# Kernel tuning notes

Hardware: AMD Instinct MI355X
Metric: run time of the kernel (lower is better)

## Reference

```python
import jax, jax.numpy as jnp
import numpy as np

B, T, E, D = 8, 2048, 2048, 256  # batch, seq (== max_seq_len), embed_size, block_size

def setup_inputs() -> dict:
    key = jax.random.key(0)
    kx, kq, kk, kv = jax.random.split(key, 4)
    x = jax.random.normal(kx, (B, T, E), dtype=jnp.float32)
    s = 1.0 / np.sqrt(E)
    Wq = jax.random.normal(kq, (E, D), dtype=jnp.float32) * s
    Wk = jax.random.normal(kk, (E, D), dtype=jnp.float32) * s
    Wv = jax.random.normal(kv, (E, D), dtype=jnp.float32) * s
    return {"x": x, "Wq": Wq, "Wk": Wk, "Wv": Wv}

def reference(x, Wq, Wk, Wv):
    # q,k,v: [B, T, D]
    q = jnp.einsum('bte,ed->btd', x, Wq)
    k = jnp.einsum('bte,ed->btd', x, Wk)
    v = jnp.einsum('bte,ed->btd', x, Wv)
    scores = jnp.einsum('bqd,bkd->bqk', q, k)  # [B, T, T]
    causal = jnp.tril(jnp.ones((T, T), dtype=bool))
    scores = jnp.where(causal, scores, -jnp.inf)
    inv_sqrt_d = 1.0 / np.sqrt(D).astype(np.float32)
    # Original divides by sqrt(D) twice: once before softmax, once inside -> net 1/D scale
    scores = scores * inv_sqrt_d
    attn = jax.nn.softmax(scores * inv_sqrt_d, axis=-1)
    z = jnp.einsum('bqk,bkd->bqd', attn, v)
    return z
```

## Files before the change

### kernel.cpp

```cpp
#include <hip/hip_runtime.h>
#include <hip/hip_bf16.h>

typedef unsigned short u16;
typedef unsigned int u32;
typedef __attribute__((ext_vector_type(8))) __bf16 bf16x8;
typedef __attribute__((ext_vector_type(4))) float f32x4;
typedef __attribute__((ext_vector_type(16))) float f32x16;
typedef __attribute__((ext_vector_type(2))) unsigned u32x2;

__device__ __forceinline__ u16 f2bf(float f) {
  u32 u = __builtin_bit_cast(u32, f);
  return (u16)((u + 0x7fffu + ((u >> 16) & 1u)) >> 16);
}
__device__ __forceinline__ float bf2f(u16 h) {
  u32 u = ((u32)h) << 16;
  return __builtin_bit_cast(float, u);
}
__device__ __forceinline__ u32 pk2(float lo, float hi) {
  union { __bf16 b[2]; u32 u; } r;
  r.b[0] = (__bf16)lo; r.b[1] = (__bf16)hi;
  return r.u;
}

__device__ __forceinline__ void pl32pair(u32& a, u32& b) {
#if __has_builtin(__builtin_amdgcn_permlane32_swap)
  u32x2 r = __builtin_amdgcn_permlane32_swap(a, b, 0, 0);
  a = r.x; b = r.y;
#else
  int hi = (int)((threadIdx.x & 63) >> 5);
  u32 as = __shfl_xor(a, 32), bs = __shfl_xor(b, 32);
  u32 na = hi ? bs : a;
  u32 nb = hi ? b : as;
  a = na; b = nb;
#endif
}
__device__ __forceinline__ float red_max32(float x) {
  u32 a = __builtin_bit_cast(u32, x), b = __builtin_bit_cast(u32, x);
  pl32pair(a, b);
  return fmaxf(__builtin_bit_cast(float, a), __builtin_bit_cast(float, b));
}
__device__ __forceinline__ float red_sum32(float x) {
  u32 a = __builtin_bit_cast(u32, x), b = __builtin_bit_cast(u32, x);
  pl32pair(a, b);
  return __builtin_bit_cast(float, a) + __builtin_bit_cast(float, b);
}

__global__ __launch_bounds__(256) void cast_x_kernel(const float* __restrict__ x,
                                                     u16* __restrict__ xb) {
  size_t i = ((size_t)blockIdx.x * 256 + threadIdx.x) * 8;
  float4 a = *(const float4*)(x + i);
  float4 b = *(const float4*)(x + i + 4);
  union { u16 h[8]; uint4 v; } o;
  o.h[0] = f2bf(a.x); o.h[1] = f2bf(a.y); o.h[2] = f2bf(a.z); o.h[3] = f2bf(a.w);
  o.h[4] = f2bf(b.x); o.h[5] = f2bf(b.y); o.h[6] = f2bf(b.z); o.h[7] = f2bf(b.w);
  *(uint4*)(xb + i) = o.v;
}

__global__ void cast_w_kernel(const float* __restrict__ Wq, const float* __restrict__ Wk,
                              const float* __restrict__ Wv, u16* __restrict__ wbt) {
  __shared__ float tile[32][33];
  int e0 = blockIdx.x * 32, d0 = blockIdx.y * 32, w = blockIdx.z;
  const float* W = (w == 0) ? Wq : ((w == 1) ? Wk : Wv);
  int x = threadIdx.x, y = threadIdx.y;
#pragma unroll
  for (int j = 0; j < 4; j++)
    tile[y + j * 8][x] = W[(size_t)(e0 + y + j * 8) * 256 + d0 + x];
  __syncthreads();
#pragma unroll
  for (int j = 0; j < 4; j++)
    wbt[(size_t)(w * 256 + d0 + y + j * 8) * 2048 + e0 + x] = f2bf(tile[x][y + j * 8]);
}

__global__ __launch_bounds__(256, 2) void gemm_kernel(const u16* __restrict__ A,
                                                      const u16* __restrict__ Bt,
                                                      u16* __restrict__ C) {
  __shared__ __align__(16) u16 As[3][4096];
  __shared__ __align__(16) u16 Bs[3][6144];

  int tid = threadIdx.x;
  int w = tid >> 6, l = tid & 63;
  int lr = l & 15, lg = l >> 4;
  int wm = w >> 1, wn = w & 1;

  int bid = blockIdx.x;
  int xcd = bid & 7;
  int colb = xcd >> 1;
  int rowb = ((xcd & 1) << 6) + (bid >> 3);
  int row0 = rowb * 128, col0 = colb * 192;

  int garow = w * 16 + (l >> 2);
  int scol = ((l & 3) * 8) ^ (((l >> 2) & 3) * 8);
  const u16* ga = A + (size_t)(row0 + garow) * 2048 + scol;
  const u16* gb = Bt + (size_t)(col0 + garow) * 2048 + scol;

  f32x4 acc[4][6];
#pragma unroll
  for (int m = 0; m < 4; m++)
#pragma unroll
    for (int n = 0; n < 6; n++) acc[m][n] = (f32x4){0.f, 0.f, 0.f, 0.f};

  int rcol = (lg * 8) ^ ((lr & 3) * 8);

#define STAGE3(ts, bi)                                                                 \
  {                                                                                    \
    _Pragma("unroll") for (int c = 0; c < 2; c++)                                      \
        __builtin_amdgcn_global_load_lds(                                              \
            (const __attribute__((address_space(1))) void*)(ga + (size_t)c * 64 * 2048 + (ts) * 32), \
            (__attribute__((address_space(3))) void*)&As[bi][(c * 64 + w * 16) * 32], 16, 0, 0); \
    _Pragma("unroll") for (int c = 0; c < 3; c++)                                      \
        __builtin_amdgcn_global_load_lds(                                              \
            (const __attribute__((address_space(1))) void*)(gb + (size_t)c * 64 * 2048 + (ts) * 32), \
            (__attribute__((address_space(3))) void*)&Bs[bi][(c * 64 + w * 16) * 32], 16, 0, 0); \
  }

  STAGE3(0, 0);
  STAGE3(1, 1);
  asm volatile("s_waitcnt vmcnt(5)" ::: "memory");
  __builtin_amdgcn_s_barrier();

  int bi = 0, bp = 2;
  for (int t = 0; t < 64; t++) {
    int ts = (t + 2 <= 63) ? (t + 2) : 63;
    const u16* asb = As[bi];
    const u16* bsb = Bs[bi];

    bf16x8 af[4], bfr[6];
#pragma unroll
    for (int m = 0; m < 4; m++)
      af[m] = *(const bf16x8*)&asb[(wm * 64 + m * 16 + lr) * 32 + rcol];
#pragma unroll
    for (int n = 0; n < 6; n++)
      bfr[n] = *(const bf16x8*)&bsb[(wn * 96 + n * 16 + lr) * 32 + rcol];

    STAGE3(ts, bp);

    asm volatile("s_waitcnt lgkmcnt(0)" ::: "memory");
    __builtin_amdgcn_sched_barrier(0);
    __builtin_amdgcn_s_setprio(1);
#pragma unroll
    for (int m = 0; m < 4; m++)
#pragma unroll
      for (int n = 0; n < 6; n++)
        acc[m][n] = __builtin_amdgcn_mfma_f32_16x16x32_bf16(af[m], bfr[n], acc[m][n], 0, 0, 0);
    __builtin_amdgcn_s_setprio(0);

    asm volatile("s_waitcnt vmcnt(5)" ::: "memory");
    __builtin_amdgcn_s_barrier();

    bi = (bi == 2) ? 0 : bi + 1;
    bp = (bp == 2) ? 0 : bp + 1;
  }
#undef STAGE3

  int crow = row0 + wm * 64;
  int ccol = col0 + wn * 96 + lr;
#pragma unroll
  for (int m = 0; m < 4; m++)
#pragma unroll
    for (int n = 0; n < 6; n++)
#pragma unroll
      for (int i = 0; i < 4; i++)
        C[(size_t)(crow + m * 16 + lg * 4 + i) * 768 + ccol + n * 16] = f2bf(acc[m][n][i]);
}

__global__ __launch_bounds__(256) void kfrag_kernel(const u16* __restrict__ qkv,
                                                    u16* __restrict__ kfrag) {
  __shared__ __align__(16) u16 tile[32 * 264];
  int t = threadIdx.x, kvb = blockIdx.x, b = blockIdx.y;
#pragma unroll
  for (int c = 0; c < 4; c++) {
    int m = c * 256 + t;
    int r = m >> 5, c16 = m & 31;
    bf16x8 v = *(const bf16x8*)(qkv + (size_t)(b * 2048 + kvb * 32 + r) * 768 + 256 + c16 * 8);
    *(bf16x8*)&tile[r * 264 + c16 * 8] = v;
  }
  __syncthreads();
#pragma unroll
  for (int c = 0; c < 4; c++) {
    int m = c * 256 + t;
    int t16 = m >> 6, l = m & 63;
    bf16x8 v = *(const bf16x8*)&tile[(l & 31) * 264 + t16 * 16 + (l >> 5) * 8];
    *(bf16x8*)(kfrag + ((size_t)((b * 64 + kvb) * 16 + t16) * 64 + l) * 8) = v;
  }
}

__global__ __launch_bounds__(256) void vfrag_kernel(const u16* __restrict__ qkv,
                                                    u16* __restrict__ vfrag) {
  __shared__ __align__(16) u16 tile[32 * 264];
  int t = threadIdx.x, kvb = blockIdx.x, b = blockIdx.y;
#pragma unroll
  for (int c = 0; c < 4; c++) {
    int m = c * 256 + t;
    int r = m >> 5, c16 = m & 31;
    bf16x8 v = *(const bf16x8*)(qkv + (size_t)(b * 2048 + kvb * 32 + r) * 768 + 512 + c16 * 8);
    *(bf16x8*)&tile[r * 264 + c16 * 8] = v;
  }
  __syncthreads();
#pragma unroll
  for (int c = 0; c < 4; c++) {
    int m = c * 256 + t;
    int ch = m >> 9, dblk = (m >> 6) & 7, l = m & 63;
    union { u16 h[8]; uint4 v; } o;
#pragma unroll
    for (int j = 0; j < 8; j++)
      o.h[j] = tile[(ch * 16 + (l >> 5) * 8 + j) * 264 + dblk * 32 + (l & 31)];
    *(uint4*)(vfrag + ((size_t)(((b * 64 + kvb) * 2 + ch) * 8 + dblk) * 64 + l) * 8) = o.v;
  }
}

__global__ __launch_bounds__(512, 2) void attn_kernel(const u16* __restrict__ qkv,
                                                      const u16* __restrict__ kfrag,
                                                      const u16* __restrict__ vfrag,
                                                      float* __restrict__ out) {
  __shared__ __align__(16) u16 qlds[16 * 512];
  __shared__ float facc[32][264];
  __shared__ float sm[4][32];
  __shared__ float sl[4][32];

  int tid = threadIdx.x;
  int w = tid >> 6, l = tid & 63;
  int ql = l & 31, hi = l >> 5;
  int stream = w & 3, dhalf = w >> 2;
  int bid = blockIdx.x;
  int b = bid & 7;
  int p = bid >> 3;

  for (int tile = 0; tile < 2; tile++) {
    int jt = tile ? p : (63 - p);
    int q0 = jt * 32;

    if (tile) __syncthreads();
#pragma unroll
    for (int c = 0; c < 2; c++) {
      int m = c * 512 + tid;
      int t16 = m >> 6, ll = m & 63;
      const u16* src = qkv + (size_t)(b * 2048 + q0 + (ll & 31)) * 768 + t16 * 16 + (ll >> 5) * 8;
      union { u16 h[8]; bf16x8 v; } in, ov;
      in.v = *(const bf16x8*)src;
#pragma unroll
      for (int j = 0; j < 8; j++) ov.h[j] = f2bf(bf2f(in.h[j]) * (1.0f / 256.0f));
      *(bf16x8*)&qlds[(t16 * 64 + ll) * 8] = ov.v;
    }
    __syncthreads();

    f32x16 o[4];
#pragma unroll
    for (int d = 0; d < 4; d++)
#pragma unroll
      for (int r = 0; r < 16; r++) o[d][r] = 0.f;
    float mreg = -__builtin_inff(), ell = 0.f;

    for (int jb = stream; jb <= jt; jb += 4) {
      const u16* kb = kfrag + ((size_t)(b * 64 + jb) * 16 * 64 + l) * 8;
      const u16* vb = vfrag + ((size_t)(b * 64 + jb) * 16 * 64 + l) * 8;

      f32x16 sA, sB;
#pragma unroll
      for (int r = 0; r < 16; r++) { sA[r] = 0.f; sB[r] = 0.f; }
#pragma unroll
      for (int g = 0; g < 4; g++) {
        bf16x8 k0 = *(const bf16x8*)(kb + (g * 4 + 0) * 512);
        bf16x8 k1 = *(const bf16x8*)(kb + (g * 4 + 1) * 512);
        bf16x8 k2 = *(const bf16x8*)(kb + (g * 4 + 2) * 512);
        bf16x8 k3 = *(const bf16x8*)(kb + (g * 4 + 3) * 512);
        bf16x8 q0f = *(const bf16x8*)&qlds[((g * 4 + 0) * 64 + l) * 8];
        bf16x8 q1f = *(const bf16x8*)&qlds[((g * 4 + 1) * 64 + l) * 8];
        bf16x8 q2f = *(const bf16x8*)&qlds[((g * 4 + 2) * 64 + l) * 8];
        bf16x8 q3f = *(const bf16x8*)&qlds[((g * 4 + 3) * 64 + l) * 8];
        sA = __builtin_amdgcn_mfma_f32_32x32x16_bf16(k0, q0f, sA, 0, 0, 0);
        sB = __builtin_amdgcn_mfma_f32_32x32x16_bf16(k1, q1f, sB, 0, 0, 0);
        sA = __builtin_amdgcn_mfma_f32_32x32x16_bf16(k2, q2f, sA, 0, 0, 0);
        sB = __builtin_amdgcn_mfma_f32_32x32x16_bf16(k3, q3f, sB, 0, 0, 0);
      }

      bf16x8 ve0[4], ve1[4];
#pragma unroll
      for (int dd = 0; dd < 4; dd++) {
        ve0[dd] = *(const bf16x8*)(vb + (dhalf * 4 + dd) * 512);
        ve1[dd] = *(const bf16x8*)(vb + (8 + dhalf * 4 + dd) * 512);
      }

      float s[16];
#pragma unroll
      for (int r = 0; r < 16; r++) s[r] = sA[r] + sB[r];

      if (jb == jt) {
#pragma unroll
        for (int r = 0; r < 16; r++) {
          int kv = (r & 3) + 8 * (r >> 2) + 4 * hi;
          if (kv > ql) s[r] = -__builtin_inff();
        }
      }

      float mx = s[0];
#pragma unroll
      for (int r = 1; r < 16; r++) mx = fmaxf(mx, s[r]);
      mx = red_max32(mx);
      if (__any(mx > mreg + 8.f)) {
        float mnew = fmaxf(mreg, mx);
        float sf = __expf(mreg - mnew);
        mreg = mnew;
        ell *= sf;
#pragma unroll
        for (int d = 0; d < 4; d++)
#pragma unroll
          for (int r = 0; r < 16; r++) o[d][r] *= sf;
      }
      float pr[16], ps = 0.f;
#pragma unroll
      for (int r = 0; r < 16; r++) { pr[r] = __expf(s[r] - mreg); ps += pr[r]; }
      ell += red_sum32(ps);

      u32 wv[8];
#pragma unroll
      for (int i = 0; i < 8; i++) wv[i] = pk2(pr[2 * i], pr[2 * i + 1]);
      pl32pair(wv[0], wv[2]); pl32pair(wv[1], wv[3]);
      pl32pair(wv[4], wv[6]); pl32pair(wv[5], wv[7]);
      union { u32 u[4]; bf16x8 v; } B0, B1;
      B0.u[0] = wv[0]; B0.u[1] = wv[1]; B0.u[2] = wv[2]; B0.u[3] = wv[3];
      B1.u[0] = wv[4]; B1.u[1] = wv[5]; B1.u[2] = wv[6]; B1.u[3] = wv[7];

#pragma unroll
      for (int dd = 0; dd < 4; dd++) {
        o[dd] = __builtin_amdgcn_mfma_f32_32x32x16_bf16(ve0[dd], B0.v, o[dd], 0, 0, 0);
        o[dd] = __builtin_amdgcn_mfma_f32_32x32x16_bf16(ve1[dd], B1.v, o[dd], 0, 0, 0);
      }
    }

    __syncthreads();
    if (w < 4 && l < 32) { sm[w][l] = mreg; sl[w][l] = ell; }
    __syncthreads();

    float M = fmaxf(fmaxf(sm[0][ql], sm[1][ql]), fmaxf(sm[2][ql], sm[3][ql]));
    float alpha = __expf(mreg - M);

#pragma unroll
    for (int ph = 0; ph < 4; ph++) {
      if (stream == ph) {
#pragma unroll
        for (int dd = 0; dd < 4; dd++)
#pragma unroll
          for (int rq = 0; rq < 4; rq++) {
            int base = (dhalf * 4 + dd) * 32 + 8 * rq + 4 * hi;
            f32x4 v;
#pragma unroll
            for (int i = 0; i < 4; i++) v[i] = alpha * o[dd][rq * 4 + i];
            float* fp = &facc[ql][base];
            if (ph == 0) *(f32x4*)fp = v;
            else {
              f32x4 old = *(const f32x4*)fp;
              *(f32x4*)fp = old + v;
            }
          }
      }
      __syncthreads();
    }

    int r = tid >> 4, lt = tid & 15;
    float Mr = fmaxf(fmaxf(sm[0][r], sm[1][r]), fmaxf(sm[2][r], sm[3][r]));
    float denom = 0.f;
#pragma unroll
    for (int ww = 0; ww < 4; ww++) denom += __expf(sm[ww][r] - Mr) * sl[ww][r];
    float inv = 1.0f / denom;
    float* orow = out + (size_t)(b * 2048 + q0 + r) * 256;
#pragma unroll
    for (int j = 0; j < 4; j++) {
      int c = (lt + j * 16) * 4;
      f32x4 v = *(const f32x4*)&facc[r][c];
      v[0] *= inv; v[1] *= inv; v[2] *= inv; v[3] *= inv;
      *(f32x4*)&orow[c] = v;
    }
  }
}

extern "C" void kernel_launch(void* const* d_in, const int* in_sizes, int n_in,
                              void* d_out, int out_size, void* d_ws, size_t ws_size,
                              hipStream_t stream) {
  (void)in_sizes; (void)n_in; (void)out_size; (void)ws_size;
  const float* x = (const float*)d_in[0];
  const float* Wq = (const float*)d_in[1];
  const float* Wk = (const float*)d_in[2];
  const float* Wv = (const float*)d_in[3];
  float* out = (float*)d_out;

  char* ws = (char*)d_ws;
  u16* xb  = (u16*)(ws);
  u16* wbt = (u16*)(ws + 67108864);
  u16* qkv = (u16*)(ws + 70254592);
  u16* kfrag = (u16*)(ws);
  u16* vfrag = (u16*)(ws + 8388608);

  cast_x_kernel<<<16384, 256, 0, stream>>>(x, xb);
  cast_w_kernel<<<dim3(64, 8, 3), dim3(32, 8), 0, stream>>>(Wq, Wk, Wv, wbt);
  gemm_kernel<<<512, 256, 0, stream>>>(xb, wbt, qkv);
  kfrag_kernel<<<dim3(64, 8), 256, 0, stream>>>(qkv, kfrag);
  vfrag_kernel<<<dim3(64, 8), 256, 0, stream>>>(qkv, vfrag);
  attn_kernel<<<256, 512, 0, stream>>>(qkv, kfrag, vfrag, out);
}
```

Baseline: 150.3 us.

## Split GEMM main loop into two MFMA phases; one attention tile per block

```diff
diff --git a/kernel.cpp b/kernel.cpp
--- a/kernel.cpp
+++ b/kernel.cpp
@@ -101,20 +101,23 @@
 
   int rcol = (lg * 8) ^ ((lr & 3) * 8);
 
-#define STAGE3(ts, bi)                                                                 \
+#define STAGE_A3(ts, bi)                                                               \
   {                                                                                    \
     _Pragma("unroll") for (int c = 0; c < 2; c++)                                      \
         __builtin_amdgcn_global_load_lds(                                              \
             (const __attribute__((address_space(1))) void*)(ga + (size_t)c * 64 * 2048 + (ts) * 32), \
             (__attribute__((address_space(3))) void*)&As[bi][(c * 64 + w * 16) * 32], 16, 0, 0); \
+  }
+#define STAGE_B3(ts, bi)                                                               \
+  {                                                                                    \
     _Pragma("unroll") for (int c = 0; c < 3; c++)                                      \
         __builtin_amdgcn_global_load_lds(                                              \
             (const __attribute__((address_space(1))) void*)(gb + (size_t)c * 64 * 2048 + (ts) * 32), \
             (__attribute__((address_space(3))) void*)&Bs[bi][(c * 64 + w * 16) * 32], 16, 0, 0); \
   }
 
-  STAGE3(0, 0);
-  STAGE3(1, 1);
+  STAGE_A3(0, 0); STAGE_B3(0, 0);
+  STAGE_A3(1, 1); STAGE_B3(1, 1);
   asm volatile("s_waitcnt vmcnt(5)" ::: "memory");
   __builtin_amdgcn_s_barrier();
 
@@ -124,33 +127,47 @@
     const u16* asb = As[bi];
     const u16* bsb = Bs[bi];
 
-    bf16x8 af[4], bfr[6];
-#pragma unroll
-    for (int m = 0; m < 4; m++)
-      af[m] = *(const bf16x8*)&asb[(wm * 64 + m * 16 + lr) * 32 + rcol];
+    bf16x8 bfr[6], af0, af1;
 #pragma unroll
     for (int n = 0; n < 6; n++)
       bfr[n] = *(const bf16x8*)&bsb[(wn * 96 + n * 16 + lr) * 32 + rcol];
-
-    STAGE3(ts, bp);
-
+    af0 = *(const bf16x8*)&asb[(wm * 64 + 0 * 16 + lr) * 32 + rcol];
+    af1 = *(const bf16x8*)&asb[(wm * 64 + 1 * 16 + lr) * 32 + rcol];
+    STAGE_A3(ts, bp);
+    __builtin_amdgcn_s_barrier();
     asm volatile("s_waitcnt lgkmcnt(0)" ::: "memory");
     __builtin_amdgcn_sched_barrier(0);
     __builtin_amdgcn_s_setprio(1);
 #pragma unroll
-    for (int m = 0; m < 4; m++)
-#pragma unroll
-      for (int n = 0; n < 6; n++)
-        acc[m][n] = __builtin_amdgcn_mfma_f32_16x16x32_bf16(af[m], bfr[n], acc[m][n], 0, 0, 0);
+    for (int n = 0; n < 6; n++) {
+      acc[0][n] = __builtin_amdgcn_mfma_f32_16x16x32_bf16(af0, bfr[n], acc[0][n], 0, 0, 0);
+      acc[1][n] = __builtin_amdgcn_mfma_f32_16x16x32_bf16(af1, bfr[n], acc[1][n], 0, 0, 0);
+    }
     __builtin_amdgcn_s_setprio(0);
-
+    __builtin_amdgcn_s_barrier();
+
+    bf16x8 af2, af3;
+    af2 = *(const bf16x8*)&asb[(wm * 64 + 2 * 16 + lr) * 32 + rcol];
+    af3 = *(const bf16x8*)&asb[(wm * 64 + 3 * 16 + lr) * 32 + rcol];
+    STAGE_B3(ts, bp);
+    __builtin_amdgcn_s_barrier();
+    asm volatile("s_waitcnt lgkmcnt(0)" ::: "memory");
+    __builtin_amdgcn_sched_barrier(0);
+    __builtin_amdgcn_s_setprio(1);
+#pragma unroll
+    for (int n = 0; n < 6; n++) {
+      acc[2][n] = __builtin_amdgcn_mfma_f32_16x16x32_bf16(af2, bfr[n], acc[2][n], 0, 0, 0);
+      acc[3][n] = __builtin_amdgcn_mfma_f32_16x16x32_bf16(af3, bfr[n], acc[3][n], 0, 0, 0);
+    }
+    __builtin_amdgcn_s_setprio(0);
     asm volatile("s_waitcnt vmcnt(5)" ::: "memory");
     __builtin_amdgcn_s_barrier();
 
     bi = (bi == 2) ? 0 : bi + 1;
     bp = (bp == 2) ? 0 : bp + 1;
   }
-#undef STAGE3
+#undef STAGE_A3
+#undef STAGE_B3
 
   int crow = row0 + wm * 64;
   int ccol = col0 + wn * 96 + lr;
@@ -208,7 +225,7 @@
   }
 }
 
-__global__ __launch_bounds__(512, 2) void attn_kernel(const u16* __restrict__ qkv,
+__global__ __launch_bounds__(512, 4) void attn_kernel(const u16* __restrict__ qkv,
                                                       const u16* __restrict__ kfrag,
                                                       const u16* __restrict__ vfrag,
                                                       float* __restrict__ out) {
@@ -223,153 +240,149 @@
   int stream = w & 3, dhalf = w >> 2;
   int bid = blockIdx.x;
   int b = bid & 7;
-  int p = bid >> 3;
-
-  for (int tile = 0; tile < 2; tile++) {
-    int jt = tile ? p : (63 - p);
-    int q0 = jt * 32;
-
-    if (tile) __syncthreads();
-#pragma unroll
-    for (int c = 0; c < 2; c++) {
-      int m = c * 512 + tid;
-      int t16 = m >> 6, ll = m & 63;
-      const u16* src = qkv + (size_t)(b * 2048 + q0 + (ll & 31)) * 768 + t16 * 16 + (ll >> 5) * 8;
-      union { u16 h[8]; bf16x8 v; } in, ov;
-      in.v = *(const bf16x8*)src;
-#pragma unroll
-      for (int j = 0; j < 8; j++) ov.h[j] = f2bf(bf2f(in.h[j]) * (1.0f / 256.0f));
-      *(bf16x8*)&qlds[(t16 * 64 + ll) * 8] = ov.v;
+  int i = bid >> 3;
+  int jt = (i & 1) ? (i >> 1) : 63 - (i >> 1);
+  int q0 = jt * 32;
+
+#pragma unroll
+  for (int c = 0; c < 2; c++) {
+    int m = c * 512 + tid;
+    int t16 = m >> 6, ll = m & 63;
+    const u16* src = qkv + (size_t)(b * 2048 + q0 + (ll & 31)) * 768 + t16 * 16 + (ll >> 5) * 8;
+    union { u16 h[8]; bf16x8 v; } in, ov;
+    in.v = *(const bf16x8*)src;
+#pragma unroll
+    for (int j = 0; j < 8; j++) ov.h[j] = f2bf(bf2f(in.h[j]) * (1.0f / 256.0f));
+    *(bf16x8*)&qlds[(t16 * 64 + ll) * 8] = ov.v;
+  }
+  __syncthreads();
+
+  f32x16 o[4];
+#pragma unroll
+  for (int d = 0; d < 4; d++)
+#pragma unroll
+    for (int r = 0; r < 16; r++) o[d][r] = 0.f;
+  float mreg = -__builtin_inff(), ell = 0.f;
+
+  for (int jb = stream; jb <= jt; jb += 4) {
+    const u16* kb = kfrag + ((size_t)(b * 64 + jb) * 16 * 64 + l) * 8;
+    const u16* vb = vfrag + ((size_t)(b * 64 + jb) * 16 * 64 + l) * 8;
+
+    f32x16 sA, sB;
+#pragma unroll
+    for (int r = 0; r < 16; r++) { sA[r] = 0.f; sB[r] = 0.f; }
+#pragma unroll
+    for (int g = 0; g < 4; g++) {
+      bf16x8 k0 = *(const bf16x8*)(kb + (g * 4 + 0) * 512);
+      bf16x8 k1 = *(const bf16x8*)(kb + (g * 4 + 1) * 512);
+      bf16x8 k2 = *(const bf16x8*)(kb + (g * 4 + 2) * 512);
+      bf16x8 k3 = *(const bf16x8*)(kb + (g * 4 + 3) * 512);
+      bf16x8 q0f = *(const bf16x8*)&qlds[((g * 4 + 0) * 64 + l) * 8];
+      bf16x8 q1f = *(const bf16x8*)&qlds[((g * 4 + 1) * 64 + l) * 8];
+      bf16x8 q2f = *(const bf16x8*)&qlds[((g * 4 + 2) * 64 + l) * 8];
+      bf16x8 q3f = *(const bf16x8*)&qlds[((g * 4 + 3) * 64 + l) * 8];
+      sA = __builtin_amdgcn_mfma_f32_32x32x16_bf16(k0, q0f, sA, 0, 0, 0);
+      sB = __builtin_amdgcn_mfma_f32_32x32x16_bf16(k1, q1f, sB, 0, 0, 0);
+      sA = __builtin_amdgcn_mfma_f32_32x32x16_bf16(k2, q2f, sA, 0, 0, 0);
+      sB = __builtin_amdgcn_mfma_f32_32x32x16_bf16(k3, q3f, sB, 0, 0, 0);
+    }
+
+    bf16x8 ve0[4], ve1[4];
+#pragma unroll
+    for (int dd = 0; dd < 4; dd++) {
+      ve0[dd] = *(const bf16x8*)(vb + (dhalf * 4 + dd) * 512);
+      ve1[dd] = *(const bf16x8*)(vb + (8 + dhalf * 4 + dd) * 512);
+    }
+
+    float s[16];
+#pragma unroll
+    for (int r = 0; r < 16; r++) s[r] = sA[r] + sB[r];
+
+    if (jb == jt) {
+#pragma unroll
+      for (int r = 0; r < 16; r++) {
+        int kv = (r & 3) + 8 * (r >> 2) + 4 * hi;
+        if (kv > ql) s[r] = -__builtin_inff();
+      }
+    }
+
+    float mx = s[0];
+#pragma unroll
+    for (int r = 1; r < 16; r++) mx = fmaxf(mx, s[r]);
+    mx = red_max32(mx);
+    if (__any(mx > mreg + 8.f)) {
+      float mnew = fmaxf(mreg, mx);
+      float sf = __expf(mreg - mnew);
+      mreg = mnew;
+      ell *= sf;
+#pragma unroll
+      for (int d = 0; d < 4; d++)
+#pragma unroll
+        for (int r = 0; r < 16; r++) o[d][r] *= sf;
+    }
+    float pr[16], ps = 0.f;
+#pragma unroll
+    for (int r = 0; r < 16; r++) { pr[r] = __expf(s[r] - mreg); ps += pr[r]; }
+    ell += red_sum32(ps);
+
+    u32 wv[8];
+#pragma unroll
+    for (int i2 = 0; i2 < 8; i2++) wv[i2] = pk2(pr[2 * i2], pr[2 * i2 + 1]);
+    pl32pair(wv[0], wv[2]); pl32pair(wv[1], wv[3]);
+    pl32pair(wv[4], wv[6]); pl32pair(wv[5], wv[7]);
+    union { u32 u[4]; bf16x8 v; } B0, B1;
+    B0.u[0] = wv[0]; B0.u[1] = wv[1]; B0.u[2] = wv[2]; B0.u[3] = wv[3];
+    B1.u[0] = wv[4]; B1.u[1] = wv[5]; B1.u[2] = wv[6]; B1.u[3] = wv[7];
+
+#pragma unroll
+    for (int dd = 0; dd < 4; dd++) {
+      o[dd] = __builtin_amdgcn_mfma_f32_32x32x16_bf16(ve0[dd], B0.v, o[dd], 0, 0, 0);
+      o[dd] = __builtin_amdgcn_mfma_f32_32x32x16_bf16(ve1[dd], B1.v, o[dd], 0, 0, 0);
+    }
+  }
+
+  __syncthreads();
+  if (w < 4 && l < 32) { sm[w][l] = mreg; sl[w][l] = ell; }
+  __syncthreads();
+
+  float M = fmaxf(fmaxf(sm[0][ql], sm[1][ql]), fmaxf(sm[2][ql], sm[3][ql]));
+  float alpha = __expf(mreg - M);
+
+#pragma unroll
+  for (int ph = 0; ph < 4; ph++) {
+    if (stream == ph) {
+#pragma unroll
+      for (int dd = 0; dd < 4; dd++)
+#pragma unroll
+        for (int rq = 0; rq < 4; rq++) {
+          int base = (dhalf * 4 + dd) * 32 + 8 * rq + 4 * hi;
+          f32x4 v;
+#pragma unroll
+          for (int i2 = 0; i2 < 4; i2++) v[i2] = alpha * o[dd][rq * 4 + i2];
+          float* fp = &facc[ql][base];
+          if (ph == 0) *(f32x4*)fp = v;
+          else {
+            f32x4 old = *(const f32x4*)fp;
+            *(f32x4*)fp = old + v;
+          }
+        }
     }
     __syncthreads();
-
-    f32x16 o[4];
-#pragma unroll
-    for (int d = 0; d < 4; d++)
-#pragma unroll
-      for (int r = 0; r < 16; r++) o[d][r] = 0.f;
-    float mreg = -__builtin_inff(), ell = 0.f;
-
-    for (int jb = stream; jb <= jt; jb += 4) {
-      const u16* kb = kfrag + ((size_t)(b * 64 + jb) * 16 * 64 + l) * 8;
-      const u16* vb = vfrag + ((size_t)(b * 64 + jb) * 16 * 64 + l) * 8;
-
-      f32x16 sA, sB;
-#pragma unroll
-      for (int r = 0; r < 16; r++) { sA[r] = 0.f; sB[r] = 0.f; }
-#pragma unroll
-      for (int g = 0; g < 4; g++) {
-        bf16x8 k0 = *(const bf16x8*)(kb + (g * 4 + 0) * 512);
-        bf16x8 k1 = *(const bf16x8*)(kb + (g * 4 + 1) * 512);
-        bf16x8 k2 = *(const bf16x8*)(kb + (g * 4 + 2) * 512);
-        bf16x8 k3 = *(const bf16x8*)(kb + (g * 4 + 3) * 512);
-        bf16x8 q0f = *(const bf16x8*)&qlds[((g * 4 + 0) * 64 + l) * 8];
-        bf16x8 q1f = *(const bf16x8*)&qlds[((g * 4 + 1) * 64 + l) * 8];
-        bf16x8 q2f = *(const bf16x8*)&qlds[((g * 4 + 2) * 64 + l) * 8];
-        bf16x8 q3f = *(const bf16x8*)&qlds[((g * 4 + 3) * 64 + l) * 8];
-        sA = __builtin_amdgcn_mfma_f32_32x32x16_bf16(k0, q0f, sA, 0, 0, 0);
-        sB = __builtin_amdgcn_mfma_f32_32x32x16_bf16(k1, q1f, sB, 0, 0, 0);
-        sA = __builtin_amdgcn_mfma_f32_32x32x16_bf16(k2, q2f, sA, 0, 0, 0);
-        sB = __builtin_amdgcn_mfma_f32_32x32x16_bf16(k3, q3f, sB, 0, 0, 0);
-      }
-
-      bf16x8 ve0[4], ve1[4];
-#pragma unroll
-      for (int dd = 0; dd < 4; dd++) {
-        ve0[dd] = *(const bf16x8*)(vb + (dhalf * 4 + dd) * 512);
-        ve1[dd] = *(const bf16x8*)(vb + (8 + dhalf * 4 + dd) * 512);
-      }
-
-      float s[16];
-#pragma unroll
-      for (int r = 0; r < 16; r++) s[r] = sA[r] + sB[r];
-
-      if (jb == jt) {
-#pragma unroll
-        for (int r = 0; r < 16; r++) {
-          int kv = (r & 3) + 8 * (r >> 2) + 4 * hi;
-          if (kv > ql) s[r] = -__builtin_inff();
-        }
-      }
-
-      float mx = s[0];
-#pragma unroll
-      for (int r = 1; r < 16; r++) mx = fmaxf(mx, s[r]);
-      mx = red_max32(mx);
-      if (__any(mx > mreg + 8.f)) {
-        float mnew = fmaxf(mreg, mx);
-        float sf = __expf(mreg - mnew);
-        mreg = mnew;
-        ell *= sf;
-#pragma unroll
-        for (int d = 0; d < 4; d++)
-#pragma unroll
-          for (int r = 0; r < 16; r++) o[d][r] *= sf;
-      }
-      float pr[16], ps = 0.f;
-#pragma unroll
-      for (int r = 0; r < 16; r++) { pr[r] = __expf(s[r] - mreg); ps += pr[r]; }
-      ell += red_sum32(ps);
-
-      u32 wv[8];
-#pragma unroll
-      for (int i = 0; i < 8; i++) wv[i] = pk2(pr[2 * i], pr[2 * i + 1]);
-      pl32pair(wv[0], wv[2]); pl32pair(wv[1], wv[3]);
-      pl32pair(wv[4], wv[6]); pl32pair(wv[5], wv[7]);
-      union { u32 u[4]; bf16x8 v; } B0, B1;
-      B0.u[0] = wv[0]; B0.u[1] = wv[1]; B0.u[2] = wv[2]; B0.u[3] = wv[3];
-      B1.u[0] = wv[4]; B1.u[1] = wv[5]; B1.u[2] = wv[6]; B1.u[3] = wv[7];
-
-#pragma unroll
-      for (int dd = 0; dd < 4; dd++) {
-        o[dd] = __builtin_amdgcn_mfma_f32_32x32x16_bf16(ve0[dd], B0.v, o[dd], 0, 0, 0);
-        o[dd] = __builtin_amdgcn_mfma_f32_32x32x16_bf16(ve1[dd], B1.v, o[dd], 0, 0, 0);
-      }
-    }
-
-    __syncthreads();
-    if (w < 4 && l < 32) { sm[w][l] = mreg; sl[w][l] = ell; }
-    __syncthreads();
-
-    float M = fmaxf(fmaxf(sm[0][ql], sm[1][ql]), fmaxf(sm[2][ql], sm[3][ql]));
-    float alpha = __expf(mreg - M);
-
-#pragma unroll
-    for (int ph = 0; ph < 4; ph++) {
-      if (stream == ph) {
-#pragma unroll
-        for (int dd = 0; dd < 4; dd++)
-#pragma unroll
-          for (int rq = 0; rq < 4; rq++) {
-            int base = (dhalf * 4 + dd) * 32 + 8 * rq + 4 * hi;
-            f32x4 v;
-#pragma unroll
-            for (int i = 0; i < 4; i++) v[i] = alpha * o[dd][rq * 4 + i];
-            float* fp = &facc[ql][base];
-            if (ph == 0) *(f32x4*)fp = v;
-            else {
-              f32x4 old = *(const f32x4*)fp;
-              *(f32x4*)fp = old + v;
-            }
-          }
-      }
-      __syncthreads();
-    }
-
-    int r = tid >> 4, lt = tid & 15;
-    float Mr = fmaxf(fmaxf(sm[0][r], sm[1][r]), fmaxf(sm[2][r], sm[3][r]));
-    float denom = 0.f;
-#pragma unroll
-    for (int ww = 0; ww < 4; ww++) denom += __expf(sm[ww][r] - Mr) * sl[ww][r];
-    float inv = 1.0f / denom;
-    float* orow = out + (size_t)(b * 2048 + q0 + r) * 256;
-#pragma unroll
-    for (int j = 0; j < 4; j++) {
-      int c = (lt + j * 16) * 4;
-      f32x4 v = *(const f32x4*)&facc[r][c];
-      v[0] *= inv; v[1] *= inv; v[2] *= inv; v[3] *= inv;
-      *(f32x4*)&orow[c] = v;
-    }
+  }
+
+  int r = tid >> 4, lt = tid & 15;
+  float Mr = fmaxf(fmaxf(sm[0][r], sm[1][r]), fmaxf(sm[2][r], sm[3][r]));
+  float denom = 0.f;
+#pragma unroll
+  for (int ww = 0; ww < 4; ww++) denom += __expf(sm[ww][r] - Mr) * sl[ww][r];
+  float inv = 1.0f / denom;
+  float* orow = out + (size_t)(b * 2048 + q0 + r) * 256;
+#pragma unroll
+  for (int j = 0; j < 4; j++) {
+    int c = (lt + j * 16) * 4;
+    f32x4 v = *(const f32x4*)&facc[r][c];
+    v[0] *= inv; v[1] *= inv; v[2] *= inv; v[3] *= inv;
+    *(f32x4*)&orow[c] = v;
   }
 }
 
@@ -395,5 +408,5 @@
   gemm_kernel<<<512, 256, 0, stream>>>(xb, wbt, qkv);
   kfrag_kernel<<<dim3(64, 8), 256, 0, stream>>>(qkv, kfrag);
   vfrag_kernel<<<dim3(64, 8), 256, 0, stream>>>(qkv, vfrag);
-  attn_kernel<<<256, 512, 0, stream>>>(qkv, kfrag, vfrag, out);
-}
+  attn_kernel<<<512, 512, 0, stream>>>(qkv, kfrag, vfrag, out);
+}
```

Measured after the change: 260.7 us. +73.4%, slower.
